# Performance work log

Hardware: AMD Instinct MI355X
Metric: run time of the kernel (lower is better)

The kernel has to match this reference:

```python
import jax, jax.numpy as jnp
import numpy as np

B, T, C = 4, 4096, 1024
H, CS = 16, 128
D = C // H
EPS = 1e-5

def _ln(x, g, b):
    m = jnp.mean(x, axis=-1, keepdims=True)
    v = jnp.var(x, axis=-1, keepdims=True)
    return (x - m) * jax.lax.rsqrt(v + EPS) * g + b

def setup_inputs() -> dict:
    key = jax.random.key(0)
    ks = jax.random.split(key, 12)
    s_c = 1.0 / np.sqrt(C)
    s_2d = 1.0 / np.sqrt(2 * D)
    return {
        "x": jax.random.normal(ks[0], (B, T, C), jnp.float32),
        "mark_W": jax.random.normal(ks[1], (C, C), jnp.float32) * s_c,
        "mark_b": jnp.zeros((C,), jnp.float32),
        "gate_W": jax.random.normal(ks[2], (C, C), jnp.float32) * s_c,
        "gate_b": jnp.zeros((C,), jnp.float32),
        "carry_g": jnp.ones((D,), jnp.float32),
        "carry_b": jnp.zeros((D,), jnp.float32),
        "card_g": jnp.ones((D,), jnp.float32),
        "card_b": jnp.zeros((D,), jnp.float32),
        "ho1_W": jax.random.normal(ks[3], (2 * D, 2 * D), jnp.float32) * s_2d,
        "ho1_b": jnp.zeros((2 * D,), jnp.float32),
        "ho2_W": jax.random.normal(ks[4], (2 * D, D), jnp.float32) * s_2d,
        "ho2_b": jnp.zeros((D,), jnp.float32),
        "proj_W": jax.random.normal(ks[5], (C, C), jnp.float32) * s_c * 0.02,
        "proj_b": jnp.zeros((C,), jnp.float32),
        "ln_g": jnp.ones((C,), jnp.float32),
        "ln_b": jnp.zeros((C,), jnp.float32),
    }

def reference(x, mark_W, mark_b, gate_W, gate_b, carry_g, carry_b,
              card_g, card_b, ho1_W, ho1_b, ho2_W, ho2_b,
              proj_W, proj_b, ln_g, ln_b):
    b, t, c = x.shape
    nc = t // CS  # T chosen divisible by chunk_size -> pad_len = 0
    pm = x @ mark_W + mark_b                       # [B,T,C]
    gates = jax.nn.sigmoid(x @ gate_W + gate_b)    # [B,T,C]

    def chunks(a):  # [B,T,C] -> [B,H,nc,CS,D]
        return a.reshape(b, nc, CS, H, D).transpose(0, 3, 1, 2, 4)

    x_h = chunks(x)
    gm = chunks(gates) * chunks(pm)                # gated marks
    lcm = jnp.cumsum(gm, axis=3)                   # local prefix sum within chunk
    chunk_sums = lcm[:, :, :, -1, :]               # [B,H,nc,D]
    carry_cum = jnp.cumsum(chunk_sums, axis=2)
    carries = jnp.concatenate(
        [jnp.zeros((b, H, 1, D), x.dtype), carry_cum[:, :, :-1, :]], axis=2)
    nrm_carry = _ln(carries, carry_g, carry_b)[:, :, :, None, :]  # [B,H,nc,1,D]
    mwc = lcm + nrm_carry                          # marks with carry
    cards_local = jnp.concatenate([nrm_carry, mwc[:, :, :, :-1, :]], axis=3)
    cards = _ln(cards_local, card_g, card_b)
    comb = jnp.concatenate([x_h, cards], axis=-1)  # [B,H,nc,CS,2D]
    h = jax.nn.gelu(comb @ ho1_W + ho1_b, approximate=False)
    ho = h @ ho2_W + ho2_b                         # [B,H,nc,CS,D]
    out = ho.transpose(0, 2, 3, 1, 4).reshape(b, t, c)
    out = out @ proj_W + proj_b
    out = _ln(out, ln_g, ln_b)
    return x + out
```

## Files before the change

### kernel.cpp

```cpp
#include <hip/hip_runtime.h>
#include <hip/hip_bf16.h>

typedef __bf16 bf16_t;
typedef __attribute__((ext_vector_type(8))) __bf16 bf16x8;
typedef __attribute__((ext_vector_type(4))) __bf16 bf16x4;
typedef __attribute__((ext_vector_type(4))) float f32x4;

static constexpr int Bn = 4, Tn = 4096, Cn = 1024, Hn = 16, CSn = 128, Dn = 64, NCn = 32;

#define DEVINL __device__ __forceinline__

DEVINL float wsum64(float v) {
  v += __shfl_xor(v, 32, 64);
  v += __shfl_xor(v, 16, 64);
  v += __shfl_xor(v, 8, 64);
  v += __shfl_xor(v, 4, 64);
  v += __shfl_xor(v, 2, 64);
  v += __shfl_xor(v, 1, 64);
  return v;
}

DEVINL float gelu_f(float v) {
  float x = v * 0.70710678f;
  float ax = fabsf(x);
  float t = 1.f / (1.f + 0.3275911f * ax);
  float poly = t * (0.254829592f +
               t * (-0.284496736f +
               t * (1.421413741f +
               t * (-1.453152027f +
               t * 1.061405429f))));
  float e = __expf(-ax * ax);
  float erfax = 1.f - poly * e;
  float erfx = copysignf(erfax, x);
  return 0.5f * v * (1.f + erfx);
}

DEVINL void gld16(const bf16_t* g, bf16_t* l) {
  __builtin_amdgcn_global_load_lds(
      (const __attribute__((address_space(1))) unsigned int*)(g),
      (__attribute__((address_space(3))) unsigned int*)(l), 16, 0, 0);
}

__global__ __launch_bounds__(256) void k_xbf(const float* __restrict__ in,
                                             bf16_t* __restrict__ out) {
  int i = blockIdx.x * 256 + threadIdx.x;
  float4 a = *reinterpret_cast<const float4*>(in + (size_t)i * 8);
  float4 b = *reinterpret_cast<const float4*>(in + (size_t)i * 8 + 4);
  bf16x8 o = {(bf16_t)a.x, (bf16_t)a.y, (bf16_t)a.z, (bf16_t)a.w,
              (bf16_t)b.x, (bf16_t)b.y, (bf16_t)b.z, (bf16_t)b.w};
  *reinterpret_cast<bf16x8*>(out + (size_t)i * 8) = o;
}

__global__ void k_transpose(const float* __restrict__ in, bf16_t* __restrict__ out,
                            int rows, int cols) {
  __shared__ float tile[64][65];
  int c0 = blockIdx.x * 64, r0 = blockIdx.y * 64;
  int tx = threadIdx.x & 63, ty = threadIdx.x >> 6;
#pragma unroll
  for (int i = ty; i < 64; i += 4)
    tile[i][tx] = in[(size_t)(r0 + i) * cols + c0 + tx];
  __syncthreads();
#pragma unroll
  for (int i = ty; i < 64; i += 4)
    out[(size_t)(c0 + i) * rows + r0 + tx] = (bf16_t)tile[tx][i];
}

__global__ __launch_bounds__(256, 2) void k_dualgemm_gm(
    const bf16_t* __restrict__ X, const bf16_t* __restrict__ Wtm,
    const bf16_t* __restrict__ Wtg, const float* __restrict__ bm,
    const float* __restrict__ bg, bf16_t* __restrict__ lcm,
    float* __restrict__ csum) {
  constexpr int K = Cn, N = Cn;
  __shared__ __align__(16) bf16_t L[6][128 * 32];
  int tid = threadIdx.x;
  int Lb = blockIdx.x + 8 * blockIdx.y;
  int xcd = Lb & 7, jj = Lb >> 3;
  int nb = jj & 7, mb = xcd + 8 * (jj >> 3);
  int m0 = mb * 128, n0 = nb * 128;
  int wave = tid >> 6, lane = tid & 63;
  int wm = wave >> 1, wn = wave & 1;
  int lr = lane & 15, lk = lane >> 4;
  int rl = lane >> 2;
  int cl = (lane & 3) * 8;
  f32x4 accP[4][4] = {};
  f32x4 accG[4][4] = {};

  const bf16_t* Xb = X + (size_t)m0 * K;
  const bf16_t* Wmb = Wtm + (size_t)n0 * K;
  const bf16_t* Wgb = Wtg + (size_t)n0 * K;

#define STAGE3(buf, kt)                                                    \
  {                                                                        \
    _Pragma("unroll")                                                      \
    for (int c = 0; c < 2; ++c) {                                          \
      int ch = wave * 2 + c;                                               \
      size_t go = (size_t)(ch * 16 + rl) * K + (kt) * 32 + cl;             \
      int lo = ch * 512;                                                   \
      gld16(Xb + go, &L[0 + (buf)][lo]);                                   \
      gld16(Wmb + go, &L[2 + (buf)][lo]);                                  \
      gld16(Wgb + go, &L[4 + (buf)][lo]);                                  \
    }                                                                      \
  }

  STAGE3(0, 0);
  __syncthreads();
  int cur = 0;
  for (int kt = 0; kt < 32; ++kt) {
    if (kt < 31) STAGE3(cur ^ 1, kt + 1);
    bf16x8 af[4], bmf[4], bgf[4];
#pragma unroll
    for (int i = 0; i < 4; ++i)
      af[i] = *reinterpret_cast<const bf16x8*>(&L[0 + cur][(wm * 64 + i * 16 + lr) * 32 + lk * 8]);
#pragma unroll
    for (int j = 0; j < 4; ++j) {
      bmf[j] = *reinterpret_cast<const bf16x8*>(&L[2 + cur][(wn * 64 + j * 16 + lr) * 32 + lk * 8]);
      bgf[j] = *reinterpret_cast<const bf16x8*>(&L[4 + cur][(wn * 64 + j * 16 + lr) * 32 + lk * 8]);
    }
#pragma unroll
    for (int i = 0; i < 4; ++i)
#pragma unroll
      for (int j = 0; j < 4; ++j) {
        accP[i][j] = __builtin_amdgcn_mfma_f32_16x16x32_bf16(af[i], bmf[j], accP[i][j], 0, 0, 0);
        accG[i][j] = __builtin_amdgcn_mfma_f32_16x16x32_bf16(af[i], bgf[j], accG[i][j], 0, 0, 0);
      }
    __syncthreads();
    cur ^= 1;
  }
#undef STAGE3

  bf16_t* G = &L[0][0];
#pragma unroll
  for (int j = 0; j < 4; ++j) {
    int col = wn * 64 + j * 16 + lr;
    float bmv = bm[n0 + col], bgv = bg[n0 + col];
#pragma unroll
    for (int i = 0; i < 4; ++i) {
      int rbase = wm * 64 + i * 16 + lk * 4;
#pragma unroll
      for (int r = 0; r < 4; ++r) {
        float p = accP[i][j][r] + bmv;
        float g = accG[i][j][r] + bgv;
        float s = 1.f / (1.f + __expf(-g));
        G[(rbase + r) * 128 + col] = (bf16_t)(s * p);
      }
    }
  }
  __syncthreads();
  if (tid < 128) {
    int col = tid;
    int bb = m0 >> 12;
    int ci = (m0 & 4095) >> 7;
    int gc = n0 + col;
    float run = 0.f;
    size_t obase = (size_t)m0 * N + gc;
#pragma unroll 8
    for (int pos = 0; pos < 128; ++pos) {
      run += (float)G[pos * 128 + col];
      lcm[obase + (size_t)pos * N] = (bf16_t)run;
    }
    csum[(((size_t)bb * Hn + (gc >> 6)) * NCn + ci) * 64 + (gc & 63)] = run;
  }
}

__global__ __launch_bounds__(64) void k_carry_ln(const float* __restrict__ csum,
                                                 float* __restrict__ ncar,
                                                 const float* __restrict__ g,
                                                 const float* __restrict__ be) {
  int bh = blockIdx.x;
  int d = threadIdx.x;
  float gd = g[d], bd = be[d];
  float run = 0.f;
  for (int ci = 0; ci < NCn; ++ci) {
    float v = run;
    run += csum[((size_t)bh * NCn + ci) * 64 + d];
    float m = wsum64(v) * (1.f / 64.f);
    float dv = v - m;
    float var = wsum64(dv * dv) * (1.f / 64.f);
    ncar[((size_t)bh * NCn + ci) * 64 + d] = dv * rsqrtf(var + 1e-5f) * gd + bd;
  }
}

__global__ __launch_bounds__(256) void k_cards_ln(const bf16_t* __restrict__ lcm,
                                                  const float* __restrict__ ncar,
                                                  const float* __restrict__ g,
                                                  const float* __restrict__ be,
                                                  bf16_t* __restrict__ cards) {
  int row = blockIdx.x * 4 + (threadIdx.x >> 6);
  int d = threadIdx.x & 63;
  int pos = row & 127, rem = row >> 7;
  int ci = rem & 31, bh = rem >> 5;
  int h = bh & 15, b = bh >> 4;
  float v = ncar[((size_t)bh * NCn + ci) * 64 + d];
  if (pos > 0)
    v += (float)lcm[((size_t)(b * Tn + ci * CSn + pos - 1)) * Cn + h * Dn + d];
  float m = wsum64(v) * (1.f / 64.f);
  float dv = v - m;
  float var = wsum64(dv * dv) * (1.f / 64.f);
  cards[(size_t)row * 64 + d] = (bf16_t)(dv * rsqrtf(var + 1e-5f) * g[d] + be[d]);
}

__global__ __launch_bounds__(256, 4) void k_ho_fused(
    const bf16_t* __restrict__ X, const bf16_t* __restrict__ cards,
    const bf16_t* __restrict__ W1t, const float* __restrict__ b1,
    const bf16_t* __restrict__ W2t, const float* __restrict__ b2,
    bf16_t* __restrict__ ho) {
  __shared__ __align__(16) bf16_t Cs[128][136];
  int tid = threadIdx.x;
  int ci = blockIdx.x & 31, bh = blockIdx.x >> 5;
  int h = bh & 15, b = bh >> 4;
  int wave = tid >> 6, lane = tid & 63;
  int wm = wave >> 1, wn = wave & 1;
  int lr = lane & 15, lk = lane >> 4;
  size_t xrow0 = (size_t)(b * Tn + ci * CSn);
#pragma unroll
  for (int i = 0; i < 4; ++i) {
    int idx = tid + 256 * i;
    int row = idx >> 3, c8 = (idx & 7) * 8;
    *reinterpret_cast<uint4*>(&Cs[row][c8]) =
        *reinterpret_cast<const uint4*>(X + (xrow0 + row) * Cn + h * Dn + c8);
  }
#pragma unroll
  for (int i = 0; i < 4; ++i) {
    int idx = tid + 256 * i;
    int row = idx >> 3, c8 = (idx & 7) * 8;
    *reinterpret_cast<uint4*>(&Cs[row][64 + c8]) =
        *reinterpret_cast<const uint4*>(cards + (((size_t)bh * NCn + ci) * CSn + row) * 64 + c8);
  }
  __syncthreads();
  f32x4 acc[4][4] = {};
#pragma unroll
  for (int ks = 0; ks < 4; ++ks) {
    bf16x8 af[4], bfr[4];
#pragma unroll
    for (int i = 0; i < 4; ++i)
      af[i] = *reinterpret_cast<const bf16x8*>(&Cs[wm * 64 + i * 16 + lr][ks * 32 + lk * 8]);
#pragma unroll
    for (int j = 0; j < 4; ++j)
      bfr[j] = *reinterpret_cast<const bf16x8*>(
          W1t + (size_t)(wn * 64 + j * 16 + lr) * 128 + ks * 32 + lk * 8);
#pragma unroll
    for (int i = 0; i < 4; ++i)
#pragma unroll
      for (int j = 0; j < 4; ++j)
        acc[i][j] = __builtin_amdgcn_mfma_f32_16x16x32_bf16(af[i], bfr[j], acc[i][j], 0, 0, 0);
  }
  __syncthreads();
#pragma unroll
  for (int j = 0; j < 4; ++j) {
    int col = wn * 64 + j * 16 + lr;
    float bv = b1[col];
#pragma unroll
    for (int i = 0; i < 4; ++i) {
      int rbase = wm * 64 + i * 16 + lk * 4;
#pragma unroll
      for (int r = 0; r < 4; ++r)
        Cs[rbase + r][col] = (bf16_t)gelu_f(acc[i][j][r] + bv);
    }
  }
  __syncthreads();
  f32x4 acc2[2][4] = {};
#pragma unroll
  for (int ks = 0; ks < 4; ++ks) {
    bf16x8 af[2], bfr[4];
#pragma unroll
    for (int i = 0; i < 2; ++i)
      af[i] = *reinterpret_cast<const bf16x8*>(&Cs[wave * 32 + i * 16 + lr][ks * 32 + lk * 8]);
#pragma unroll
    for (int j = 0; j < 4; ++j)
      bfr[j] = *reinterpret_cast<const bf16x8*>(
          W2t + (size_t)(j * 16 + lr) * 128 + ks * 32 + lk * 8);
#pragma unroll
    for (int i = 0; i < 2; ++i)
#pragma unroll
      for (int j = 0; j < 4; ++j)
        acc2[i][j] = __builtin_amdgcn_mfma_f32_16x16x32_bf16(af[i], bfr[j], acc2[i][j], 0, 0, 0);
  }
#pragma unroll
  for (int j = 0; j < 4; ++j) {
    int dd = j * 16 + lr;
    float bv = b2[dd];
#pragma unroll
    for (int i = 0; i < 2; ++i) {
      int pbase = wave * 32 + i * 16 + lk * 4;
#pragma unroll
      for (int r = 0; r < 4; ++r)
        ho[(xrow0 + pbase + r) * Cn + h * Dn + dd] = (bf16_t)(acc2[i][j][r] + bv);
    }
  }
}

__global__ __launch_bounds__(256, 2) void k_gemm_bt(
    const bf16_t* __restrict__ A, const bf16_t* __restrict__ Wt,
    const float* __restrict__ bias, bf16_t* __restrict__ out) {
  constexpr int K = Cn, N = Cn;
  __shared__ __align__(16) bf16_t L[4][128 * 32];
  int tid = threadIdx.x;
  int Lb = blockIdx.x + 8 * blockIdx.y;
  int xcd = Lb & 7, jj = Lb >> 3;
  int nb = jj & 7, mb = xcd + 8 * (jj >> 3);
  int m0 = mb * 128, n0 = nb * 128;
  int wave = tid >> 6, lane = tid & 63;
  int wm = wave >> 1, wn = wave & 1;
  int lr = lane & 15, lk = lane >> 4;
  int rl = lane >> 2, cl = (lane & 3) * 8;
  f32x4 acc[4][4] = {};
  const bf16_t* Ab = A + (size_t)m0 * K;
  const bf16_t* Wb = Wt + (size_t)n0 * K;

#define STAGE2(buf, kt)                                                    \
  {                                                                        \
    _Pragma("unroll")                                                      \
    for (int c = 0; c < 2; ++c) {                                          \
      int ch = wave * 2 + c;                                               \
      size_t go = (size_t)(ch * 16 + rl) * K + (kt) * 32 + cl;             \
      int lo = ch * 512;                                                   \
      gld16(Ab + go, &L[0 + (buf)][lo]);                                   \
      gld16(Wb + go, &L[2 + (buf)][lo]);                                   \
    }                                                                      \
  }

  STAGE2(0, 0);
  __syncthreads();
  int cur = 0;
  for (int kt = 0; kt < 32; ++kt) {
    if (kt < 31) STAGE2(cur ^ 1, kt + 1);
    bf16x8 af[4], bfr[4];
#pragma unroll
    for (int i = 0; i < 4; ++i)
      af[i] = *reinterpret_cast<const bf16x8*>(&L[0 + cur][(wm * 64 + i * 16 + lr) * 32 + lk * 8]);
#pragma unroll
    for (int j = 0; j < 4; ++j)
      bfr[j] = *reinterpret_cast<const bf16x8*>(&L[2 + cur][(wn * 64 + j * 16 + lr) * 32 + lk * 8]);
#pragma unroll
    for (int i = 0; i < 4; ++i)
#pragma unroll
      for (int j = 0; j < 4; ++j)
        acc[i][j] = __builtin_amdgcn_mfma_f32_16x16x32_bf16(af[i], bfr[j], acc[i][j], 0, 0, 0);
    __syncthreads();
    cur ^= 1;
  }
#undef STAGE2
#pragma unroll
  for (int j = 0; j < 4; ++j) {
    int col = n0 + wn * 64 + j * 16 + lr;
    float bv = bias[col];
#pragma unroll
    for (int i = 0; i < 4; ++i) {
      int rbase = m0 + wm * 64 + i * 16 + lk * 4;
#pragma unroll
      for (int r = 0; r < 4; ++r)
        out[(size_t)(rbase + r) * N + col] = (bf16_t)(acc[i][j][r] + bv);
    }
  }
}

__global__ __launch_bounds__(256) void k_ln_residual(
    const bf16_t* __restrict__ pre, const float* __restrict__ X,
    const float* __restrict__ g, const float* __restrict__ be,
    float* __restrict__ out) {
  int row = blockIdx.x, t = threadIdx.x;
  size_t base = (size_t)row * Cn + t * 4;
  bf16x4 pv4 = *reinterpret_cast<const bf16x4*>(pre + base);
  float v0 = (float)pv4[0], v1 = (float)pv4[1], v2 = (float)pv4[2], v3 = (float)pv4[3];
  float s = v0 + v1 + v2 + v3;
  float q = v0 * v0 + v1 * v1 + v2 * v2 + v3 * v3;
  s = wsum64(s);
  q = wsum64(q);
  __shared__ float red[8];
  int wv = t >> 6, ln = t & 63;
  if (ln == 0) { red[wv] = s; red[4 + wv] = q; }
  __syncthreads();
  float tot = red[0] + red[1] + red[2] + red[3];
  float totq = red[4] + red[5] + red[6] + red[7];
  float mean = tot * (1.f / 1024.f);
  float var = totq * (1.f / 1024.f) - mean * mean;
  float rs = rsqrtf(fmaxf(var, 0.f) + 1e-5f);
  float4 xv = *reinterpret_cast<const float4*>(X + base);
  float4 gv = *reinterpret_cast<const float4*>(g + t * 4);
  float4 bv = *reinterpret_cast<const float4*>(be + t * 4);
  float4 o;
  o.x = (v0 - mean) * rs * gv.x + bv.x + xv.x;
  o.y = (v1 - mean) * rs * gv.y + bv.y + xv.y;
  o.z = (v2 - mean) * rs * gv.z + bv.z + xv.z;
  o.w = (v3 - mean) * rs * gv.w + bv.w + xv.w;
  *reinterpret_cast<float4*>(out + base) = o;
}

extern "C" void kernel_launch(void* const* d_in, const int* in_sizes, int n_in,
                              void* d_out, int out_size, void* d_ws, size_t ws_size,
                              hipStream_t stream) {
  const float* x       = (const float*)d_in[0];
  const float* mark_W  = (const float*)d_in[1];
  const float* mark_b  = (const float*)d_in[2];
  const float* gate_W  = (const float*)d_in[3];
  const float* gate_b  = (const float*)d_in[4];
  const float* carry_g = (const float*)d_in[5];
  const float* carry_b = (const float*)d_in[6];
  const float* card_g  = (const float*)d_in[7];
  const float* card_b  = (const float*)d_in[8];
  const float* ho1_W   = (const float*)d_in[9];
  const float* ho1_b   = (const float*)d_in[10];
  const float* ho2_W   = (const float*)d_in[11];
  const float* ho2_b   = (const float*)d_in[12];
  const float* proj_W  = (const float*)d_in[13];
  const float* proj_b  = (const float*)d_in[14];
  const float* ln_g    = (const float*)d_in[15];
  const float* ln_b    = (const float*)d_in[16];
  float* out = (float*)d_out;

  char* ws = (char*)d_ws;
  bf16_t* xbf    = (bf16_t*)(ws + 0);
  bf16_t* outpre = (bf16_t*)(ws + 0);
  bf16_t* gm     = (bf16_t*)(ws + 33554432);
  bf16_t* cards  = (bf16_t*)(ws + 67108864);
  bf16_t* hobuf  = (bf16_t*)(ws + 100663296);
  float*  csum   = (float*)(ws + 134217728);
  float*  ncar   = (float*)(ws + 134742016);
  bf16_t* wtm    = (bf16_t*)(ws + 135266304);
  bf16_t* wtg    = (bf16_t*)(ws + 137363456);
  bf16_t* wtp    = (bf16_t*)(ws + 139460608);
  bf16_t* wt1    = (bf16_t*)(ws + 141557760);
  bf16_t* wt2    = (bf16_t*)(ws + 141590528);

  k_xbf<<<8192, 256, 0, stream>>>(x, xbf);
  k_transpose<<<dim3(16, 16), 256, 0, stream>>>(mark_W, wtm, 1024, 1024);
  k_transpose<<<dim3(16, 16), 256, 0, stream>>>(gate_W, wtg, 1024, 1024);
  k_transpose<<<dim3(16, 16), 256, 0, stream>>>(proj_W, wtp, 1024, 1024);
  k_transpose<<<dim3(2, 2),   256, 0, stream>>>(ho1_W, wt1, 128, 128);
  k_transpose<<<dim3(1, 2),   256, 0, stream>>>(ho2_W, wt2, 128, 64);

  k_dualgemm_gm<<<dim3(8, 128), 256, 0, stream>>>(xbf, wtm, wtg, mark_b, gate_b, gm, csum);
  k_carry_ln<<<64, 64, 0, stream>>>(csum, ncar, carry_g, carry_b);
  k_cards_ln<<<65536, 256, 0, stream>>>(gm, ncar, card_g, card_b, cards);
  k_ho_fused<<<2048, 256, 0, stream>>>(xbf, cards, wt1, ho1_b, wt2, ho2_b, hobuf);
  k_gemm_bt<<<dim3(8, 128), 256, 0, stream>>>(hobuf, wtp, proj_b, outpre);
  k_ln_residual<<<16384, 256, 0, stream>>>(outpre, x, ln_g, ln_b, out);
}
```

Before: 294.6 us.

## Fuse cards LayerNorm into head-output kernel and pad gated-mark LDS stride

Removes the standalone cards LayerNorm kernel. Each head-output block now reads the shifted local prefix sums and the normalized carry directly and computes the per-row LayerNorm into shared memory, with 8 lanes per row and shuffle reductions. This avoids writing and re-reading the full cards intermediate in global memory and saves one large launch. Separately, the gated-mark staging tile in the dual GEMM uses a row stride of 132 instead of 128 to reduce LDS bank conflicts. The fused LayerNorm computes variance as E[x²]−mean², which is slightly less numerically robust than the two-pass form.

New measurement: 250.8 us. 14.9% less time.

```diff
diff --git a/kernel.cpp b/kernel.cpp
--- a/kernel.cpp
+++ b/kernel.cpp
@@ -71,6 +71,7 @@
     const float* __restrict__ bg, bf16_t* __restrict__ lcm,
     float* __restrict__ csum) {
   constexpr int K = Cn, N = Cn;
+  constexpr int GP = 132;
   __shared__ __align__(16) bf16_t L[6][128 * 32];
   int tid = threadIdx.x;
   int Lb = blockIdx.x + 8 * blockIdx.y;
@@ -141,7 +142,7 @@
         float p = accP[i][j][r] + bmv;
         float g = accG[i][j][r] + bgv;
         float s = 1.f / (1.f + __expf(-g));
-        G[(rbase + r) * 128 + col] = (bf16_t)(s * p);
+        G[(rbase + r) * GP + col] = (bf16_t)(s * p);
       }
     }
   }
@@ -155,7 +156,7 @@
     size_t obase = (size_t)m0 * N + gc;
 #pragma unroll 8
     for (int pos = 0; pos < 128; ++pos) {
-      run += (float)G[pos * 128 + col];
+      run += (float)G[pos * GP + col];
       lcm[obase + (size_t)pos * N] = (bf16_t)run;
     }
     csum[(((size_t)bb * Hn + (gc >> 6)) * NCn + ci) * 64 + (gc & 63)] = run;
@@ -180,30 +181,12 @@
   }
 }
 
-__global__ __launch_bounds__(256) void k_cards_ln(const bf16_t* __restrict__ lcm,
-                                                  const float* __restrict__ ncar,
-                                                  const float* __restrict__ g,
-                                                  const float* __restrict__ be,
-                                                  bf16_t* __restrict__ cards) {
-  int row = blockIdx.x * 4 + (threadIdx.x >> 6);
-  int d = threadIdx.x & 63;
-  int pos = row & 127, rem = row >> 7;
-  int ci = rem & 31, bh = rem >> 5;
-  int h = bh & 15, b = bh >> 4;
-  float v = ncar[((size_t)bh * NCn + ci) * 64 + d];
-  if (pos > 0)
-    v += (float)lcm[((size_t)(b * Tn + ci * CSn + pos - 1)) * Cn + h * Dn + d];
-  float m = wsum64(v) * (1.f / 64.f);
-  float dv = v - m;
-  float var = wsum64(dv * dv) * (1.f / 64.f);
-  cards[(size_t)row * 64 + d] = (bf16_t)(dv * rsqrtf(var + 1e-5f) * g[d] + be[d]);
-}
-
 __global__ __launch_bounds__(256, 4) void k_ho_fused(
-    const bf16_t* __restrict__ X, const bf16_t* __restrict__ cards,
-    const bf16_t* __restrict__ W1t, const float* __restrict__ b1,
-    const bf16_t* __restrict__ W2t, const float* __restrict__ b2,
-    bf16_t* __restrict__ ho) {
+    const bf16_t* __restrict__ X, const bf16_t* __restrict__ lcm,
+    const float* __restrict__ ncar, const float* __restrict__ cg,
+    const float* __restrict__ cb, const bf16_t* __restrict__ W1t,
+    const float* __restrict__ b1, const bf16_t* __restrict__ W2t,
+    const float* __restrict__ b2, bf16_t* __restrict__ ho) {
   __shared__ __align__(16) bf16_t Cs[128][136];
   int tid = threadIdx.x;
   int ci = blockIdx.x & 31, bh = blockIdx.x >> 5;
@@ -219,12 +202,46 @@
     *reinterpret_cast<uint4*>(&Cs[row][c8]) =
         *reinterpret_cast<const uint4*>(X + (xrow0 + row) * Cn + h * Dn + c8);
   }
-#pragma unroll
-  for (int i = 0; i < 4; ++i) {
-    int idx = tid + 256 * i;
-    int row = idx >> 3, c8 = (idx & 7) * 8;
-    *reinterpret_cast<uint4*>(&Cs[row][64 + c8]) =
-        *reinterpret_cast<const uint4*>(cards + (((size_t)bh * NCn + ci) * CSn + row) * 64 + c8);
+  {
+    int lg = lane >> 3;
+    int le = lane & 7;
+    int d0 = le * 8;
+    const float* np = ncar + ((size_t)bh * NCn + ci) * 64 + d0;
+    float ncv[8], ggv[8], bbv[8];
+#pragma unroll
+    for (int e = 0; e < 8; ++e) {
+      ncv[e] = np[e];
+      ggv[e] = cg[d0 + e];
+      bbv[e] = cb[d0 + e];
+    }
+#pragma unroll
+    for (int it = 0; it < 4; ++it) {
+      int pr = wave * 32 + it * 8 + lg;
+      float v[8];
+      if (pr > 0) {
+        bf16x8 lv = *reinterpret_cast<const bf16x8*>(
+            lcm + (xrow0 + pr - 1) * Cn + h * Dn + d0);
+#pragma unroll
+        for (int e = 0; e < 8; ++e) v[e] = (float)lv[e] + ncv[e];
+      } else {
+#pragma unroll
+        for (int e = 0; e < 8; ++e) v[e] = ncv[e];
+      }
+      float s = 0.f, q = 0.f;
+#pragma unroll
+      for (int e = 0; e < 8; ++e) { s += v[e]; q += v[e] * v[e]; }
+      s += __shfl_xor(s, 1, 64); q += __shfl_xor(q, 1, 64);
+      s += __shfl_xor(s, 2, 64); q += __shfl_xor(q, 2, 64);
+      s += __shfl_xor(s, 4, 64); q += __shfl_xor(q, 4, 64);
+      float mean = s * (1.f / 64.f);
+      float var = q * (1.f / 64.f) - mean * mean;
+      float rs = rsqrtf(fmaxf(var, 0.f) + 1e-5f);
+      bf16x8 o;
+#pragma unroll
+      for (int e = 0; e < 8; ++e)
+        o[e] = (bf16_t)((v[e] - mean) * rs * ggv[e] + bbv[e]);
+      *reinterpret_cast<bf16x8*>(&Cs[pr][64 + d0]) = o;
+    }
   }
   __syncthreads();
   f32x4 acc[4][4] = {};
@@ -412,7 +429,6 @@
   bf16_t* xbf    = (bf16_t*)(ws + 0);
   bf16_t* outpre = (bf16_t*)(ws + 0);
   bf16_t* gm     = (bf16_t*)(ws + 33554432);
-  bf16_t* cards  = (bf16_t*)(ws + 67108864);
   bf16_t* hobuf  = (bf16_t*)(ws + 100663296);
   float*  csum   = (float*)(ws + 134217728);
   float*  ncar   = (float*)(ws + 134742016);
@@ -431,8 +447,8 @@
 
   k_dualgemm_gm<<<dim3(8, 128), 256, 0, stream>>>(xbf, wtm, wtg, mark_b, gate_b, gm, csum);
   k_carry_ln<<<64, 64, 0, stream>>>(csum, ncar, carry_g, carry_b);
-  k_cards_ln<<<65536, 256, 0, stream>>>(gm, ncar, card_g, card_b, cards);
-  k_ho_fused<<<2048, 256, 0, stream>>>(xbf, cards, wt1, ho1_b, wt2, ho2_b, hobuf);
+  k_ho_fused<<<2048, 256, 0, stream>>>(xbf, gm, ncar, card_g, card_b,
+                                       wt1, ho1_b, wt2, ho2_b, hobuf);
   k_gemm_bt<<<dim3(8, 128), 256, 0, stream>>>(hobuf, wtp, proj_b, outpre);
   k_ln_residual<<<16384, 256, 0, stream>>>(outpre, x, ln_g, ln_b, out);
 }
```
